# Kernel optimization log

Measured on AMD Instinct MI355X. Metric: run time of the kernel, lower is better.

The kernel has to match this reference:

```python
import jax, jax.numpy as jnp
import numpy as np
import math

B, C, W, H = 4, 64, 128, 128
S = 2                 # len(shifts)
SHIFTS = (1, 2)       # dilations
HC = C // S           # hidden_channels = 32
NL = 8                # num_layer (8 diff stencils)
AREA = W * H
EPS = 1e-5


def _base_kernels():
    # 4 forward diff stencils + their 180-degree flips (delta2 = delta1[:, :, ::-1, ::-1])
    d1 = np.array([[[-1, 0, 0], [0, 1, 0], [0, 0, 0]],
                   [[0, -1, 0], [0, 1, 0], [0, 0, 0]],
                   [[0, 0, -1], [0, 1, 0], [0, 0, 0]],
                   [[0, 0, 0], [0, 1, -1], [0, 0, 0]]], dtype=np.float32).reshape(4, 1, 3, 3)
    d2 = d1[:, :, ::-1, ::-1].copy()
    return np.concatenate([d1, d2], axis=0)  # (8, 1, 3, 3)

# Depthwise kernel: per input channel, all 8 stencils (feature_group_count=HC layout)
_DW_KERNEL = jnp.asarray(np.tile(_base_kernels()[None], (HC, 1, 1, 1, 1)).reshape(NL * HC, 1, 3, 3))


def setup_inputs() -> dict:
    key = jax.random.key(0)
    ks = jax.random.split(key, 6)
    s = 0.05
    return {
        "x": jax.random.normal(ks[0], (B, C, W, H), jnp.float32),
        "trans_w": jax.random.normal(ks[1], (C, C), jnp.float32) * s,
        "bn1_g": jnp.ones((C,), jnp.float32),
        "bn1_b": jnp.zeros((C,), jnp.float32),
        "query_w": jax.random.normal(ks[2], (S, HC, HC), jnp.float32) * s,
        "key_w": jax.random.normal(ks[3], (S, (NL + 1) * HC, (NL + 1) * HC), jnp.float32) * s,
        "out_w": jax.random.normal(ks[4], (C, C), jnp.float32) * s,
        "bn2_g": jnp.ones((C,), jnp.float32),
        "bn2_b": jnp.zeros((C,), jnp.float32),
    }


def _bn_relu(y, g, b):
    # train-mode BatchNorm2d (biased batch stats) + ReLU
    m = y.mean((0, 2, 3), keepdims=True)
    v = y.var((0, 2, 3), keepdims=True)
    return jax.nn.relu((y - m) * jax.lax.rsqrt(v + EPS) * g[None, :, None, None] + b[None, :, None, None])


def _dw_diff_convs(x, dil):
    # x: (B, HC, W, H) -> 8 depthwise dilated 3x3 diff convs, concat order kernel-major
    y = jax.lax.conv_general_dilated(
        x, _DW_KERNEL, window_strides=(1, 1), padding='SAME',
        rhs_dilation=(dil, dil), feature_group_count=HC,
        dimension_numbers=('NCHW', 'OIHW', 'NCHW'))
    # grouped layout is (channel, stencil); torch concat order is (stencil, channel)
    return y.reshape(B, HC, NL, W, H).transpose(0, 2, 1, 3, 4).reshape(B, NL * HC, W, H)


def _inorm(w):
    # InstanceNorm2d(affine=False) over the last two dims, per (batch, shift)
    m = w.mean((-2, -1), keepdims=True)
    v = w.var((-2, -1), keepdims=True)
    return (w - m) * jax.lax.rsqrt(v + EPS)


def _l2n(x):
    # F.normalize(dim=-1)
    n = jnp.linalg.norm(x, axis=-1, keepdims=True)
    return x / jnp.maximum(n, 1e-12)


def reference(x, trans_w, bn1_g, bn1_b, query_w, key_w, out_w, bn2_g, bn2_b):
    y = _bn_relu(jnp.einsum('bchw,oc->bohw', x, trans_w), bn1_g, bn1_b)
    cens = y.reshape(B, S, HC, W, H)  # torch.chunk along channels
    keys, qrys, svs = [], [], []
    for i in range(S):
        c = cens[:, i]
        sur = _dw_diff_convs(c, SHIFTS[i])                                      # (B, 8*HC, W, H)
        kk = jnp.einsum('bchw,oc->bohw', jnp.concatenate([sur, c], 1), key_w[i])
        qq = jnp.einsum('bchw,oc->bohw', c, query_w[i])
        keys.append(kk.reshape(B, (NL + 1) * HC, AREA))
        qrys.append(qq.reshape(B, HC, AREA))
        svs.append(sur.reshape(B, NL * HC, AREA))
    keys = _l2n(jnp.stack(keys, 1))     # (B, S, 9*HC, AREA)
    qrys = _l2n(jnp.stack(qrys, 1))     # (B, S, HC, AREA)
    svs = jnp.stack(svs, 1)             # (B, S, 8*HC, AREA)
    w = jnp.einsum('bsca,bska->bsck', qrys, keys) / math.sqrt(AREA)  # (B, S, HC, 9*HC)
    sw = jax.nn.softmax(_inorm(w[..., :NL * HC]), axis=-1)           # (B, S, HC, 8*HC)
    out = jnp.einsum('bsck,bska->bsca', sw, svs).reshape(B, C, W, H)
    return _bn_relu(jnp.einsum('bchw,oc->bohw', out, out_w), bn2_g, bn2_b)
```

## Files before the change

kernel.cpp:

```cpp
#include <hip/hip_runtime.h>

#define BB 4
#define CC 64
#define SS 2
#define HCC 32
#define AREA_ 16384
#define KDIM 288
#define YPITCH 44

typedef _Float16 half8 __attribute__((ext_vector_type(8)));
typedef float f32x16 __attribute__((ext_vector_type(16)));

static __device__ __forceinline__ float warp_rsum(float v){
#pragma unroll
  for (int o=32;o>0;o>>=1) v += __shfl_down(v,o,64);
  return v;
}
static __device__ __forceinline__ float warp_rmax(float v){
#pragma unroll
  for (int o=32;o>0;o>>=1) v = fmaxf(v,__shfl_down(v,o,64));
  return v;
}

__global__ __launch_bounds__(256) void conv64_kernel(const float* __restrict__ in,
    const float* __restrict__ wmat, float* __restrict__ out){
  int b = blockIdx.x >> 7;
  int p0 = (blockIdx.x & 127) << 7;
  __shared__ float tile[64][132];
  __shared__ float wsm[64][68];
  for (int idx = threadIdx.x; idx < 4096; idx += 256){
    int c = idx & 63, o = idx >> 6;
    wsm[c][o] = wmat[o*64 + c];
  }
  const float* inb = in + (size_t)b*CC*AREA_ + p0;
  for (int idx = threadIdx.x; idx < 8192; idx += 256){
    int c = idx >> 7, pp = idx & 127;
    tile[c][pp] = inb[(size_t)c*AREA_ + pp];
  }
  __syncthreads();
  int px = (threadIdx.x & 31) * 4;
  int og = threadIdx.x >> 5;
  float4 acc[8];
#pragma unroll
  for (int i=0;i<8;i++) acc[i] = make_float4(0.f,0.f,0.f,0.f);
  for (int c=0;c<64;c++){
    float4 v  = *(const float4*)&tile[c][px];
    float4 w0 = *(const float4*)&wsm[c][og*8];
    float4 w1 = *(const float4*)&wsm[c][og*8+4];
    float wv[8] = {w0.x,w0.y,w0.z,w0.w,w1.x,w1.y,w1.z,w1.w};
#pragma unroll
    for (int i=0;i<8;i++){
      acc[i].x = fmaf(wv[i], v.x, acc[i].x);
      acc[i].y = fmaf(wv[i], v.y, acc[i].y);
      acc[i].z = fmaf(wv[i], v.z, acc[i].z);
      acc[i].w = fmaf(wv[i], v.w, acc[i].w);
    }
  }
  float* ob = out + (size_t)b*CC*AREA_ + p0 + px;
#pragma unroll
  for (int i=0;i<8;i++)
    *(float4*)&ob[(size_t)(og*8+i)*AREA_] = acc[i];
}

__global__ __launch_bounds__(256) void bn_part_kernel(const float* __restrict__ src,
    float* __restrict__ part){
  int c = blockIdx.x, chunk = blockIdx.y;
  float s1=0.f, s2=0.f;
  for (int b=0;b<BB;b++){
    const float* p = src + ((size_t)b*CC + c)*AREA_ + chunk*2048;
    for (int i=threadIdx.x;i<2048;i+=256){ float v=p[i]; s1+=v; s2+=v*v; }
  }
  __shared__ float red[8];
  float w1 = warp_rsum(s1), w2 = warp_rsum(s2);
  int lane = threadIdx.x & 63, wid = threadIdx.x >> 6;
  if (lane==0){ red[wid]=w1; red[4+wid]=w2; }
  __syncthreads();
  if (threadIdx.x==0){
    atomicAdd(&part[c], red[0]+red[1]+red[2]+red[3]);
    atomicAdd(&part[64+c], red[4]+red[5]+red[6]+red[7]);
  }
}

__global__ __launch_bounds__(256) void bn_apply_relu_kernel(const float* __restrict__ src,
    const float* __restrict__ part, const float* __restrict__ gam,
    const float* __restrict__ bet, float* __restrict__ dst){
  size_t i = (size_t)blockIdx.x*256 + threadIdx.x;
  int c = (int)((i >> 14) & 63);
  const float N = (float)(BB*AREA_);
  float m = part[c]/N;
  float var = part[64+c]/N - m*m;
  float sc = gam[c]*rsqrtf(var + 1e-5f);
  float bi = bet[c] - m*sc;
  float v = fmaf(src[i], sc, bi);
  dst[i] = v > 0.f ? v : 0.f;
}

__global__ __launch_bounds__(256) void qq_kernel(const float* __restrict__ y,
    const float* __restrict__ qw, float* __restrict__ qq){
  int blk = blockIdx.x;
  int p0 = (blk & 127) << 7;
  int s = (blk >> 7) & 1;
  int b = blk >> 8;
  __shared__ float tile[32][132];
  __shared__ float wsm[32][36];
  const float* qws = qw + s*HCC*HCC;
  for (int idx=threadIdx.x; idx<1024; idx+=256){
    int c = idx & 31, o = idx >> 5;
    wsm[c][o] = qws[o*32 + c];
  }
  const float* yb = y + ((size_t)b*CC + s*HCC)*AREA_ + p0;
  for (int idx=threadIdx.x; idx<4096; idx+=256){
    int c=idx>>7, pp=idx&127;
    tile[c][pp] = yb[(size_t)c*AREA_ + pp];
  }
  __syncthreads();
  int px = (threadIdx.x & 31) * 4;
  int og = threadIdx.x >> 5;
  float4 acc[4];
#pragma unroll
  for (int i=0;i<4;i++) acc[i] = make_float4(0.f,0.f,0.f,0.f);
  for (int c=0;c<32;c++){
    float4 v  = *(const float4*)&tile[c][px];
    float4 w0 = *(const float4*)&wsm[c][og*4];
    float wv[4] = {w0.x,w0.y,w0.z,w0.w};
#pragma unroll
    for (int i=0;i<4;i++){
      acc[i].x = fmaf(wv[i], v.x, acc[i].x);
      acc[i].y = fmaf(wv[i], v.y, acc[i].y);
      acc[i].z = fmaf(wv[i], v.z, acc[i].z);
      acc[i].w = fmaf(wv[i], v.w, acc[i].w);
    }
  }
  float* ob = qq + ((size_t)(b*SS+s)*HCC)*AREA_ + p0 + px;
#pragma unroll
  for (int i=0;i<4;i++)
    *(float4*)&ob[(size_t)(og*4+i)*AREA_] = acc[i];
}

__global__ __launch_bounds__(512) void gram_kernel(const float* __restrict__ y,
    const float* __restrict__ qq, float* __restrict__ dpart, float* __restrict__ wpart){
  const int PAarr[6]={0,0,1,0,1,2}, PBarr[6]={0,1,1,2,2,2};
  const int pairOrder[6]={1,3,4,0,2,5};
  const int pairbase[6]={0,262144,524288,786432,917504,1048576};
  const int tsz[6]={16384,16384,16384,8192,8192,4096};
  int bid = blockIdx.x;
  int bs = bid & 7;
  int sidx = bid >> 3;
  int pair = pairOrder[sidx >> 4];
  int slotIdx = sidx & 15;
  int Kstart = slotIdx << 10;
  const int nch = 16;
  int PA = PAarr[pair], PB = PBarr[pair];
  int RA = PA<2?128:64, CB = PB<2?128:64;
  bool diag = (PA==PB);
  int rows_tot = RA + (diag?0:CB);
  int passes = rows_tot >> 6;
  int s = bs & 1, b = bs >> 1, dil = 1+s;
  const float* yb = y + ((size_t)b*CC + s*HCC)*AREA_;
  const float* qqb = qq + (size_t)bs*HCC*AREA_;
  __shared__ __align__(16) _Float16 Us[256*64];
  int tid = threadIdx.x;
  int hq = tid & 7, rr8 = tid >> 3;
  int lane = tid & 63, wid = tid >> 6;
  int rbase = (wid>>2)*64, cbase = (wid&3)*32;
  bool active = (rbase < RA) && (cbase < CB);
  int boff = diag ? 0 : RA;
  int r0 = rbase + (lane&31), r1 = r0+32;
  int cr = boff + cbase + (lane&31);
  int uo = lane>>5;

  auto loadPass = [&](int t, int p)->half8{
    int k0 = Kstart + t*64;
    int w = k0>>7, h = (k0&127) + hq*8;
    int pr = p*64 + rr8;
    int pan, prow;
    if (pr < RA){ pan = PA; prow = pr; } else { pan = PB; prow = pr - RA; }
    float vv[8];
    if (pan < 2){
      int l = pan*4 + (prow>>5), ch = prow & 31;
      int oy = ((0x6A40 >> (2*l)) & 3) - 1;
      int ox = ((0x6A4  >> (2*l)) & 3) - 1;
      const float* crow = yb + (size_t)ch*AREA_ + w*128 + h;
      float4 ca = *(const float4*)crow;
      float4 cb = *(const float4*)(crow+4);
      float cen[8] = {ca.x,ca.y,ca.z,ca.w,cb.x,cb.y,cb.z,cb.w};
      float nb[8];
      int wy = w + oy*dil, oxd = ox*dil, hb = h + oxd;
      if (wy>=0 && wy<128){
        const float* nrow = yb + (size_t)ch*AREA_ + wy*128 + hb;
        if (hb>=0 && hb<=120){
          float4 na, nc;
          __builtin_memcpy(&na, nrow, 16);
          __builtin_memcpy(&nc, nrow+4, 16);
          nb[0]=na.x; nb[1]=na.y; nb[2]=na.z; nb[3]=na.w;
          nb[4]=nc.x; nb[5]=nc.y; nb[6]=nc.z; nb[7]=nc.w;
        } else {
#pragma unroll
          for (int j=0;j<8;j++){
            int hx = hb + j;
            nb[j] = (hx>=0 && hx<128) ? nrow[j] : 0.f;
          }
        }
      } else {
#pragma unroll
        for (int j=0;j<8;j++) nb[j]=0.f;
      }
#pragma unroll
      for (int j=0;j<8;j++) vv[j] = cen[j]-nb[j];
    } else {
      const float* src = (prow<32) ? yb + (size_t)prow*AREA_ : qqb + (size_t)(prow-32)*AREA_;
      const float* crow = src + w*128 + h;
      float4 ca = *(const float4*)crow;
      float4 cb = *(const float4*)(crow+4);
      vv[0]=ca.x; vv[1]=ca.y; vv[2]=ca.z; vv[3]=ca.w;
      vv[4]=cb.x; vv[5]=cb.y; vv[6]=cb.z; vv[7]=cb.w;
    }
    half8 hv;
#pragma unroll
    for (int j=0;j<8;j++) hv[j] = (_Float16)vv[j];
    return hv;
  };
  auto writeLDS = [&](int p, half8 hv){
    int pr = p*64 + rr8;
    *(half8*)&Us[(size_t)pr*64 + ((hq ^ (pr&7))<<3)] = hv;
  };

  bool p2 = (passes >= 2), p3 = (passes >= 3), p4 = (passes >= 4);
  half8 f0{}, f1{}, f2{}, f3{};

  f32x16 acc0={}, acc1={};
  f0 = loadPass(0,0);
  if (p2) f1 = loadPass(0,1);
  if (p3) f2 = loadPass(0,2);
  if (p4) f3 = loadPass(0,3);
  for (int t=0; t<nch; ++t){
    asm volatile("s_waitcnt lgkmcnt(0)" ::: "memory");
    __builtin_amdgcn_s_barrier();
    writeLDS(0,f0);
    if (p2) writeLDS(1,f1);
    if (p3) writeLDS(2,f2);
    if (p4) writeLDS(3,f3);
    if (t+1 < nch){
      f0 = loadPass(t+1,0);
      if (p2) f1 = loadPass(t+1,1);
      if (p3) f2 = loadPass(t+1,2);
      if (p4) f3 = loadPass(t+1,3);
    }
    asm volatile("s_waitcnt lgkmcnt(0)" ::: "memory");
    __builtin_amdgcn_s_barrier();
    if (active){
#pragma unroll
      for (int st=0; st<4; ++st){
        int u = st*2 + uo;
        half8 a0 = *(const half8*)&Us[(size_t)r0*64 + ((u^(r0&7))<<3)];
        half8 a1 = *(const half8*)&Us[(size_t)r1*64 + ((u^(r1&7))<<3)];
        half8 bb = *(const half8*)&Us[(size_t)cr*64 + ((u^(cr&7))<<3)];
        acc0 = __builtin_amdgcn_mfma_f32_32x32x16_f16(a0,bb,acc0,0,0,0);
        acc1 = __builtin_amdgcn_mfma_f32_32x32x16_f16(a1,bb,acc1,0,0,0);
      }
    }
  }
  if (active){
    size_t off = (size_t)bs*1114112 + pairbase[pair] + (size_t)slotIdx*tsz[pair];
    float* pp = (off < 4194304) ? (dpart + off) : (wpart + (off - 4194304));
    int cp = (pair<3)?128:64;
    int rr = 4*uo, cc = lane&31;
#pragma unroll
    for (int reg=0;reg<16;reg++){
      int ro = (reg&3) + 8*(reg>>2) + rr;
      pp[(size_t)(rbase+ro)*cp + cbase+cc]    = acc0[reg];
      pp[(size_t)(rbase+32+ro)*cp + cbase+cc] = acc1[reg];
    }
  }
}

__global__ __launch_bounds__(256) void reduce_kernel(const float* __restrict__ dpart,
    const float* __restrict__ wpart, float* __restrict__ P){
  const int PAarr[6]={0,0,1,0,1,2}, PBarr[6]={0,1,1,2,2,2};
  const int pairbase[6]={0,262144,524288,786432,917504,1048576};
  const int tsz[6]={16384,16384,16384,8192,8192,4096};
  const int chunkbase[7]={0,16,32,48,56,64,68};
  int chunk = blockIdx.x, bs = blockIdx.y;
  int pair = 0;
  while (chunk >= chunkbase[pair+1]) pair++;
  int lc = chunk - chunkbase[pair];
  int CN = (pair<3)?128:64;
  int Roff = PAarr[pair]*128, Coff = PBarr[pair]*128;
  int csh = (CN==128)?7:6;
  int cell0 = lc*1024 + threadIdx.x*4;
  int r = cell0 >> csh, c = cell0 & (CN-1);
  float4 v = make_float4(0.f,0.f,0.f,0.f);
  size_t base = (size_t)bs*1114112 + pairbase[pair];
  for (int k=0;k<16;k++){
    size_t off = base + (size_t)k*tsz[pair];
    const float* pp = (off < 4194304) ? (dpart + off) : (wpart + (off - 4194304));
    float4 t = *(const float4*)&pp[(size_t)r*CN + c];
    v.x += t.x; v.y += t.y; v.z += t.z; v.w += t.w;
  }
  float* Pb = P + (size_t)bs*102400;
  *(float4*)&Pb[(size_t)(Roff+r)*320 + Coff+c] = v;
  Pb[(size_t)(Coff+c  )*320 + Roff+r] = v.x;
  Pb[(size_t)(Coff+c+1)*320 + Roff+r] = v.y;
  Pb[(size_t)(Coff+c+2)*320 + Roff+r] = v.z;
  Pb[(size_t)(Coff+c+3)*320 + Roff+r] = v.w;
}

__global__ __launch_bounds__(256) void kwT_kernel(const float* __restrict__ kw, float* __restrict__ kwT){
  int idx = blockIdx.x*256 + threadIdx.x;
  if (idx >= 2*KDIM*KDIM) return;
  int s = idx / (KDIM*KDIM);
  int r = idx - s*KDIM*KDIM;
  int k = r / KDIM, j = r - k*KDIM;
  kwT[(size_t)s*KDIM*KDIM + (size_t)j*KDIM + k] = kw[idx];
}

__global__ __launch_bounds__(256) void vknorm_kernel(const float* __restrict__ P,
    const float* __restrict__ kwT, float* __restrict__ kn){
  int j = blockIdx.x, bs = blockIdx.y;
  int s = bs & 1;
  __shared__ float prow[KDIM];
  const float* Pb = P + (size_t)bs*102400 + (size_t)j*320;
  for (int i=threadIdx.x;i<KDIM;i+=256) prow[i]=Pb[i];
  __syncthreads();
  const float* kt = kwT + (size_t)s*KDIM*KDIM;
  int k = threadIdx.x;
  float acc=0.f;
  for (int jp=0;jp<KDIM;jp++) acc = fmaf(prow[jp], kt[(size_t)jp*KDIM + k], acc);
  atomicAdd(&kn[bs*256 + k], kt[(size_t)j*KDIM + k] * acc);
}

__global__ __launch_bounds__(256) void wmat_kernel(const float* __restrict__ P,
    const float* __restrict__ kwT, const float* __restrict__ kn,
    float* __restrict__ wbuf, float* __restrict__ wstats){
  int bs = blockIdx.x >> 5, c = blockIdx.x & 31;
  int s = bs & 1;
  __shared__ float prow[KDIM];
  const float* PbB = P + (size_t)bs*102400;
  const float* Pb = PbB + (size_t)(288+c)*320;
  for (int i=threadIdx.x;i<KDIM;i+=256) prow[i]=Pb[i];
  __syncthreads();
  const float* kt = kwT + (size_t)s*KDIM*KDIM;
  int k = threadIdx.x;
  float acc=0.f;
  for (int j=0;j<KDIM;j++) acc = fmaf(prow[j], kt[(size_t)j*KDIM + k], acc);
  float rk = 1.f/fmaxf(sqrtf(fmaxf(kn[bs*256+k],0.f)),1e-12f);
  float qn = PbB[(size_t)(288+c)*320 + 288+c];
  float rq = 1.f/fmaxf(sqrtf(fmaxf(qn,0.f)),1e-12f);
  float wv = acc * rq * rk * (1.f/128.f);
  wbuf[((size_t)bs*32 + c)*256 + k] = wv;
  __shared__ float red[8];
  float r1 = warp_rsum(wv), r2 = warp_rsum(wv*wv);
  int lane = threadIdx.x & 63, wid = threadIdx.x >> 6;
  if (lane==0){ red[wid]=r1; red[4+wid]=r2; }
  __syncthreads();
  if (threadIdx.x==0){
    atomicAdd(&wstats[bs*2],   red[0]+red[1]+red[2]+red[3]);
    atomicAdd(&wstats[bs*2+1], red[4]+red[5]+red[6]+red[7]);
  }
}

__global__ __launch_bounds__(256) void smx_kernel(const float* __restrict__ wbuf,
    const float* __restrict__ wstats, float* __restrict__ sw){
  int bs = blockIdx.x >> 5, c = blockIdx.x & 31;
  float s1 = wstats[bs*2], s2 = wstats[bs*2+1];
  const float N = 8192.f;
  float m = s1/N, var = s2/N - m*m;
  float rs = rsqrtf(var + 1e-5f);
  int k = threadIdx.x;
  float v = (wbuf[((size_t)bs*32 + c)*256 + k] - m)*rs;
  __shared__ float red[4];
  float mx = warp_rmax(v);
  int lane = k & 63, wid = k >> 6;
  if (lane==0) red[wid]=mx;
  __syncthreads();
  float MX = fmaxf(fmaxf(red[0],red[1]),fmaxf(red[2],red[3]));
  __syncthreads();
  float e = expf(v - MX);
  float es = warp_rsum(e);
  if (lane==0) red[wid]=es;
  __syncthreads();
  float ES = red[0]+red[1]+red[2]+red[3];
  sw[((size_t)bs*32 + c)*256 + k] = e/ES;
}

__global__ __launch_bounds__(256) void tswf_kernel(const float* __restrict__ sw, _Float16* __restrict__ tswf){
  int idx = blockIdx.x*256 + threadIdx.x;
  if (idx >= 9216) return;
  int lane = idx & 63;
  int ks = (idx >> 6) % 18;
  int bs = idx / (18*64);
  int c = lane & 31;
  const float* swb = sw + ((size_t)bs*32 + c)*256;
  half8 hv;
#pragma unroll
  for (int j=0;j<8;j++){
    int k = ks*16 + ((lane>>5)<<3) + j;
    int t = k >> 5, ch = k & 31;
    float v;
    if (t==0){ v=0.f; for (int l=0;l<8;l++) v += swb[l*32+ch]; }
    else v = -swb[(t-1)*32 + ch];
    hv[j] = (_Float16)v;
  }
  *(half8*)&tswf[(size_t)idx*8] = hv;
}

__global__ __launch_bounds__(256,2) void attn_mfma_kernel(const float* __restrict__ y,
    const _Float16* __restrict__ tswf, float* __restrict__ outs){
  int blk = blockIdx.x;
  int w = blk & 127;
  int s = (blk >> 7) & 1;
  int b = blk >> 8;
  int bs = b*SS + s;
  int dil = 1 + s;
  __shared__ __align__(16) _Float16 ybuf[3*132*YPITCH];
  const float* yb = y + ((size_t)bs*HCC)*AREA_;
  int tid = threadIdx.x;
  int lane = tid & 63, wid = tid >> 6;

  const _Float16* tf = tswf + ((size_t)bs*18*64 + lane)*8;
  half8 afr[18];
#pragma unroll
  for (int ks=0; ks<18; ++ks) afr[ks] = *(const half8*)&tf[(size_t)ks*64*8];

  for (int i = tid; i < 384; i += 256){
    int ch = i & 31;
    int q = i >> 5;
    int wr = q >> 2, hb = q & 3;
    int hi = (hb < 2) ? hb : (128 + hb);
    int oct = (ch>>3) ^ ((hi>>2)&3);
    ybuf[(size_t)(wr*132+hi)*YPITCH + oct*8 + (ch&7)] = (_Float16)0.f;
  }
  int ch8 = tid >> 5;
  int h4 = (tid & 31) * 4;
#pragma unroll
  for (int r = 0; r < 12; ++r){
    int wr = r >> 2, chg = r & 3;
    int wy = w + (wr-1)*dil;
    if (wy < 0 || wy >= 128) continue;
    int ch = chg*8 + ch8;
    float4 v = *(const float4*)&yb[(size_t)ch*AREA_ + wy*128 + h4];
    float vv[4] = {v.x, v.y, v.z, v.w};
#pragma unroll
    for (int j=0;j<4;j++){
      int hi = h4 + 2 + j;
      int oct = (ch>>3) ^ ((hi>>2)&3);
      ybuf[(size_t)(wr*132+hi)*YPITCH + oct*8 + (ch&7)] = (_Float16)vv[j];
    }
  }
  __syncthreads();

  const int offy[9]={0,-1,-1,-1,0,1,1,1,0};
  const int offx[9]={0,-1,0,1,1,1,0,-1,-1};
  int n0 = wid * 32;
  int nl = n0 + (lane & 31);
  int ko = lane >> 5;
  f32x16 acc = {};
#pragma unroll
  for (int ks=0; ks<18; ++ks){
    int t = ks >> 1;
    int wy = w + offy[t]*dil;
    half8 bfr = {};
    if (wy >= 0 && wy < 128){
      int wr = offy[t] + 1;
      int hi = nl + offx[t]*dil + 2;
      int oct = (((ks&1)<<1) | ko) ^ ((hi>>2)&3);
      bfr = *(const half8*)&ybuf[(size_t)(wr*132+hi)*YPITCH + oct*8];
    }
    acc = __builtin_amdgcn_mfma_f32_32x32x16_f16(afr[ks], bfr, acc, 0,0,0);
  }
  float* ob = outs + (size_t)bs*HCC*AREA_ + (size_t)w*128;
  int col = n0 + (lane & 31);
  int rb = 4*(lane>>5);
#pragma unroll
  for (int reg=0; reg<16; ++reg){
    int c = (reg&3) + 8*(reg>>2) + rb;
    ob[(size_t)c*AREA_ + col] = acc[reg];
  }
}

extern "C" void kernel_launch(void* const* d_in, const int* in_sizes, int n_in,
                              void* d_out, int out_size, void* d_ws, size_t ws_size,
                              hipStream_t stream){
  const float* x   = (const float*)d_in[0];
  const float* tw  = (const float*)d_in[1];
  const float* g1  = (const float*)d_in[2];
  const float* b1  = (const float*)d_in[3];
  const float* qw  = (const float*)d_in[4];
  const float* kw  = (const float*)d_in[5];
  const float* ow  = (const float*)d_in[6];
  const float* g2  = (const float*)d_in[7];
  const float* b2  = (const float*)d_in[8];
  float* out = (float*)d_out;
  float* ws = (float*)d_ws;

  float* y      = ws + 64;
  float* qqb    = ws + 4194368;
  float* kwT    = qqb;
  float* wbuf   = ws + 4360256;
  float* wpart  = ws + 8388672;
  float* outs   = wpart;
  float* P      = ws + 13107264;
  float* stats  = ws + 13926464;
  float* wstats = ws + 13926720;
  float* kn     = ws + 13926976;
  float* swb    = ws + 13929280;
  _Float16* tswf = (_Float16*)(ws + 13994816);
  float* dpart  = (float*)d_out;
  float* z      = y;

  hipMemsetAsync(stats, 0, 2560*sizeof(float), stream);

  conv64_kernel<<<512,256,0,stream>>>(x, tw, y);
  bn_part_kernel<<<dim3(64,8),256,0,stream>>>(y, stats);
  bn_apply_relu_kernel<<<16384,256,0,stream>>>(y, stats, g1, b1, y);
  qq_kernel<<<1024,256,0,stream>>>(y, qw, qqb);
  gram_kernel<<<768,512,0,stream>>>(y, qqb, dpart, wpart);
  reduce_kernel<<<dim3(68,8),256,0,stream>>>(dpart, wpart, P);
  kwT_kernel<<<648,256,0,stream>>>(kw, kwT);
  vknorm_kernel<<<dim3(288,8),256,0,stream>>>(P, kwT, kn);
  wmat_kernel<<<256,256,0,stream>>>(P, kwT, kn, wbuf, wstats);
  smx_kernel<<<256,256,0,stream>>>(wbuf, wstats, swb);
  tswf_kernel<<<36,256,0,stream>>>(swb, tswf);
  attn_mfma_kernel<<<1024,256,0,stream>>>(y, tswf, outs);
  conv64_kernel<<<512,256,0,stream>>>(outs, ow, z);
  bn_part_kernel<<<dim3(64,8),256,0,stream>>>(z, stats+128);
  bn_apply_relu_kernel<<<16384,256,0,stream>>>(z, stats+128, g2, b2, out);
}
```

Measured before the change: 249.8 us.

## Fuse BN statistics into conv epilogue, BN-apply with query conv, softmax with tswf

The 1x1 conv kernels now reduce per-channel sum and sum-of-squares in their epilogue through warp shuffles and atomics, which removes both standalone BN-statistics passes. The first BN apply+ReLU is fused with the query projection for both shifts in one kernel that writes y and qq together. The softmax kernel also builds the fp16 transformed weights directly, dropping the separate tswf kernel and its intermediate buffer. This cuts several full-tensor reads and kernel launches, at the cost of more atomics and a larger conv epilogue.

Measured after the change: 395.9 us. 1.59x slower.

```diff
diff --git a/kernel.cpp b/kernel.cpp
--- a/kernel.cpp
+++ b/kernel.cpp
@@ -23,7 +23,7 @@
 }
 
 __global__ __launch_bounds__(256) void conv64_kernel(const float* __restrict__ in,
-    const float* __restrict__ wmat, float* __restrict__ out){
+    const float* __restrict__ wmat, float* __restrict__ out, float* __restrict__ part){
   int b = blockIdx.x >> 7;
   int p0 = (blockIdx.x & 127) << 7;
   __shared__ float tile[64][132];
@@ -60,24 +60,26 @@
 #pragma unroll
   for (int i=0;i<8;i++)
     *(float4*)&ob[(size_t)(og*8+i)*AREA_] = acc[i];
-}
-
-__global__ __launch_bounds__(256) void bn_part_kernel(const float* __restrict__ src,
-    float* __restrict__ part){
-  int c = blockIdx.x, chunk = blockIdx.y;
-  float s1=0.f, s2=0.f;
-  for (int b=0;b<BB;b++){
-    const float* p = src + ((size_t)b*CC + c)*AREA_ + chunk*2048;
-    for (int i=threadIdx.x;i<2048;i+=256){ float v=p[i]; s1+=v; s2+=v*v; }
-  }
-  __shared__ float red[8];
-  float w1 = warp_rsum(s1), w2 = warp_rsum(s2);
-  int lane = threadIdx.x & 63, wid = threadIdx.x >> 6;
-  if (lane==0){ red[wid]=w1; red[4+wid]=w2; }
-  __syncthreads();
-  if (threadIdx.x==0){
-    atomicAdd(&part[c], red[0]+red[1]+red[2]+red[3]);
-    atomicAdd(&part[64+c], red[4]+red[5]+red[6]+red[7]);
+  float s1[8], s2[8];
+#pragma unroll
+  for (int i=0;i<8;i++){
+    s1[i] = acc[i].x+acc[i].y+acc[i].z+acc[i].w;
+    s2[i] = acc[i].x*acc[i].x+acc[i].y*acc[i].y+acc[i].z*acc[i].z+acc[i].w*acc[i].w;
+  }
+#pragma unroll
+  for (int o=16;o>0;o>>=1){
+#pragma unroll
+    for (int i=0;i<8;i++){
+      s1[i] += __shfl_down(s1[i], o, 32);
+      s2[i] += __shfl_down(s2[i], o, 32);
+    }
+  }
+  if ((threadIdx.x & 31) == 0){
+#pragma unroll
+    for (int i=0;i<8;i++){
+      atomicAdd(&part[og*8+i], s1[i]);
+      atomicAdd(&part[64+og*8+i], s2[i]);
+    }
   }
 }
 
@@ -95,46 +97,65 @@
   dst[i] = v > 0.f ? v : 0.f;
 }
 
-__global__ __launch_bounds__(256) void qq_kernel(const float* __restrict__ y,
-    const float* __restrict__ qw, float* __restrict__ qq){
-  int blk = blockIdx.x;
-  int p0 = (blk & 127) << 7;
-  int s = (blk >> 7) & 1;
-  int b = blk >> 8;
-  __shared__ float tile[32][132];
-  __shared__ float wsm[32][36];
-  const float* qws = qw + s*HCC*HCC;
-  for (int idx=threadIdx.x; idx<1024; idx+=256){
+__global__ __launch_bounds__(256) void bnqq_kernel(const float* __restrict__ ycv,
+    const float* __restrict__ part, const float* __restrict__ gam,
+    const float* __restrict__ bet, const float* __restrict__ qw,
+    float* __restrict__ y, float* __restrict__ qq){
+  int b = blockIdx.x >> 7;
+  int p0 = (blockIdx.x & 127) << 7;
+  __shared__ float tile[64][132];
+  __shared__ float wsmT[32][68];
+  __shared__ float scs[64], bis[64];
+  int tid = threadIdx.x;
+  for (int idx = tid; idx < 2048; idx += 256){
     int c = idx & 31, o = idx >> 5;
-    wsm[c][o] = qws[o*32 + c];
-  }
-  const float* yb = y + ((size_t)b*CC + s*HCC)*AREA_ + p0;
-  for (int idx=threadIdx.x; idx<4096; idx+=256){
-    int c=idx>>7, pp=idx&127;
-    tile[c][pp] = yb[(size_t)c*AREA_ + pp];
-  }
-  __syncthreads();
-  int px = (threadIdx.x & 31) * 4;
-  int og = threadIdx.x >> 5;
-  float4 acc[4];
-#pragma unroll
-  for (int i=0;i<4;i++) acc[i] = make_float4(0.f,0.f,0.f,0.f);
+    wsmT[c][o] = qw[(o>>5)*1024 + (o&31)*32 + c];
+  }
+  if (tid < 64){
+    const float N = (float)(BB*AREA_);
+    float m = part[tid]/N;
+    float var = part[64+tid]/N - m*m;
+    float sc = gam[tid]*rsqrtf(var + 1e-5f);
+    scs[tid] = sc;
+    bis[tid] = bet[tid] - m*sc;
+  }
+  __syncthreads();
+  const float* inb = ycv + (size_t)b*CC*AREA_ + p0;
+  float* yb = y + (size_t)b*CC*AREA_ + p0;
+  for (int idx = tid; idx < 8192; idx += 256){
+    int c = idx >> 7, pp = idx & 127;
+    float v = fmaf(inb[(size_t)c*AREA_ + pp], scs[c], bis[c]);
+    v = v > 0.f ? v : 0.f;
+    tile[c][pp] = v;
+    yb[(size_t)c*AREA_ + pp] = v;
+  }
+  __syncthreads();
+  int px = (tid & 31) * 4;
+  int og = tid >> 5;
+  int sBase = (og >= 4) ? 32 : 0;
+  float4 acc[8];
+#pragma unroll
+  for (int i=0;i<8;i++) acc[i] = make_float4(0.f,0.f,0.f,0.f);
   for (int c=0;c<32;c++){
-    float4 v  = *(const float4*)&tile[c][px];
-    float4 w0 = *(const float4*)&wsm[c][og*4];
-    float wv[4] = {w0.x,w0.y,w0.z,w0.w};
-#pragma unroll
-    for (int i=0;i<4;i++){
+    float4 v  = *(const float4*)&tile[sBase+c][px];
+    float4 w0 = *(const float4*)&wsmT[c][og*8];
+    float4 w1 = *(const float4*)&wsmT[c][og*8+4];
+    float wv[8] = {w0.x,w0.y,w0.z,w0.w,w1.x,w1.y,w1.z,w1.w};
+#pragma unroll
+    for (int i=0;i<8;i++){
       acc[i].x = fmaf(wv[i], v.x, acc[i].x);
       acc[i].y = fmaf(wv[i], v.y, acc[i].y);
       acc[i].z = fmaf(wv[i], v.z, acc[i].z);
       acc[i].w = fmaf(wv[i], v.w, acc[i].w);
     }
   }
-  float* ob = qq + ((size_t)(b*SS+s)*HCC)*AREA_ + p0 + px;
-#pragma unroll
-  for (int i=0;i<4;i++)
-    *(float4*)&ob[(size_t)(og*4+i)*AREA_] = acc[i];
+#pragma unroll
+  for (int i=0;i<8;i++){
+    int o = og*8 + i;
+    int s = o >> 5, oc = o & 31;
+    float* ob = qq + (((size_t)(b*SS+s)*HCC + oc)*AREA_) + p0 + px;
+    *(float4*)ob = acc[i];
+  }
 }
 
 __global__ __launch_bounds__(512) void gram_kernel(const float* __restrict__ y,
@@ -359,8 +380,8 @@
   }
 }
 
-__global__ __launch_bounds__(256) void smx_kernel(const float* __restrict__ wbuf,
-    const float* __restrict__ wstats, float* __restrict__ sw){
+__global__ __launch_bounds__(256) void smxtswf_kernel(const float* __restrict__ wbuf,
+    const float* __restrict__ wstats, _Float16* __restrict__ tswf){
   int bs = blockIdx.x >> 5, c = blockIdx.x & 31;
   float s1 = wstats[bs*2], s2 = wstats[bs*2+1];
   const float N = 8192.f;
@@ -369,6 +390,8 @@
   int k = threadIdx.x;
   float v = (wbuf[((size_t)bs*32 + c)*256 + k] - m)*rs;
   __shared__ float red[4];
+  __shared__ float sm[256];
+  __shared__ float cs[32];
   float mx = warp_rmax(v);
   int lane = k & 63, wid = k >> 6;
   if (lane==0) red[wid]=mx;
@@ -380,28 +403,29 @@
   if (lane==0) red[wid]=es;
   __syncthreads();
   float ES = red[0]+red[1]+red[2]+red[3];
-  sw[((size_t)bs*32 + c)*256 + k] = e/ES;
-}
-
-__global__ __launch_bounds__(256) void tswf_kernel(const float* __restrict__ sw, _Float16* __restrict__ tswf){
-  int idx = blockIdx.x*256 + threadIdx.x;
-  if (idx >= 9216) return;
-  int lane = idx & 63;
-  int ks = (idx >> 6) % 18;
-  int bs = idx / (18*64);
-  int c = lane & 31;
-  const float* swb = sw + ((size_t)bs*32 + c)*256;
-  half8 hv;
-#pragma unroll
-  for (int j=0;j<8;j++){
-    int k = ks*16 + ((lane>>5)<<3) + j;
-    int t = k >> 5, ch = k & 31;
-    float v;
-    if (t==0){ v=0.f; for (int l=0;l<8;l++) v += swb[l*32+ch]; }
-    else v = -swb[(t-1)*32 + ch];
-    hv[j] = (_Float16)v;
-  }
-  *(half8*)&tswf[(size_t)idx*8] = hv;
+  sm[k] = e/ES;
+  __syncthreads();
+  if (k < 32){
+    float a = 0.f;
+#pragma unroll
+    for (int l=0;l<8;l++) a += sm[l*32+k];
+    cs[k] = a;
+  }
+  __syncthreads();
+  if (k < 36){
+    int ks = k >> 1;
+    int hi = k & 1;
+    int ln = c + (hi<<5);
+    half8 hv;
+#pragma unroll
+    for (int j=0;j<8;j++){
+      int ki = ks*16 + (hi<<3) + j;
+      int t = ki >> 5, ch = ki & 31;
+      float vv = (t==0) ? cs[ch] : -sm[(t-1)*32 + ch];
+      hv[j] = (_Float16)vv;
+    }
+    *(half8*)&tswf[((size_t)(bs*18 + ks)*64 + ln)*8] = hv;
+  }
 }
 
 __global__ __launch_bounds__(256,2) void attn_mfma_kernel(const float* __restrict__ y,
@@ -503,26 +527,21 @@
   float* stats  = ws + 13926464;
   float* wstats = ws + 13926720;
   float* kn     = ws + 13926976;
-  float* swb    = ws + 13929280;
   _Float16* tswf = (_Float16*)(ws + 13994816);
   float* dpart  = (float*)d_out;
   float* z      = y;
 
   hipMemsetAsync(stats, 0, 2560*sizeof(float), stream);
 
-  conv64_kernel<<<512,256,0,stream>>>(x, tw, y);
-  bn_part_kernel<<<dim3(64,8),256,0,stream>>>(y, stats);
-  bn_apply_relu_kernel<<<16384,256,0,stream>>>(y, stats, g1, b1, y);
-  qq_kernel<<<1024,256,0,stream>>>(y, qw, qqb);
+  conv64_kernel<<<512,256,0,stream>>>(x, tw, y, stats);
+  bnqq_kernel<<<512,256,0,stream>>>(y, stats, g1, b1, qw, y, qqb);
   gram_kernel<<<768,512,0,stream>>>(y, qqb, dpart, wpart);
   reduce_kernel<<<dim3(68,8),256,0,stream>>>(dpart, wpart, P);
   kwT_kernel<<<648,256,0,stream>>>(kw, kwT);
   vknorm_kernel<<<dim3(288,8),256,0,stream>>>(P, kwT, kn);
   wmat_kernel<<<256,256,0,stream>>>(P, kwT, kn, wbuf, wstats);
-  smx_kernel<<<256,256,0,stream>>>(wbuf, wstats, swb);
-  tswf_kernel<<<36,256,0,stream>>>(swb, tswf);
+  smxtswf_kernel<<<256,256,0,stream>>>(wbuf, wstats, tswf);
   attn_mfma_kernel<<<1024,256,0,stream>>>(y, tswf, outs);
-  conv64_kernel<<<512,256,0,stream>>>(outs, ow, z);
-  bn_part_kernel<<<dim3(64,8),256,0,stream>>>(z, stats+128);
+  conv64_kernel<<<512,256,0,stream>>>(outs, ow, z, stats+128);
   bn_apply_relu_kernel<<<16384,256,0,stream>>>(z, stats+128, g2, b2, out);
 }
```
